# Kernel optimization log

Measured on AMD Instinct MI355X. Metric: run time of the kernel, lower is better.

The kernel has to match this reference:

```python
import jax, jax.numpy as jnp
import numpy as np
from jax import lax

K = 17  # depthwise conv kernel size (MossFormer ConvModule)
DIM = 512
HID = 2048      # dim * expansion_factor(4)
DQK = 128
GRP = 256       # group_size


def layernorm(x, g, b, eps=1e-5):
    mu = x.mean(-1, keepdims=True)
    var = ((x - mu) ** 2).mean(-1, keepdims=True)
    return (x - mu) * lax.rsqrt(var + eps) * g + b


def dwconv_res(h, dw):
    # h: [b, n, c]; dw: [K, c] depthwise kernel; residual connection, SAME padding
    c = h.shape[-1]
    conv = lax.conv_general_dilated(h, dw[:, None, :], (1,), 'SAME',
                                    dimension_numbers=('NWC', 'WIO', 'NWC'),
                                    feature_group_count=c)
    return h + conv


def ffconvm(x, ln_g, ln_b, W, b, dw):
    h = jax.nn.silu(layernorm(x, ln_g, ln_b) @ W + b)
    return dwconv_res(h, dw)


def setup_inputs() -> dict:
    key = jax.random.key(0)
    ks = jax.random.split(key, 16)
    r = lambda k, shape, s=0.02: (jax.random.normal(k, shape, dtype=jnp.float32) * s)
    inp = {
        'x': jax.random.normal(ks[0], (8, 2048, DIM), dtype=jnp.float32),
        # to_hidden FFConvM: LN(dim) -> Linear(dim, HID) -> SiLU -> depthwise conv residual
        'ln_h_g': jnp.ones((DIM,), jnp.float32), 'ln_h_b': jnp.zeros((DIM,), jnp.float32),
        'W_h': r(ks[1], (DIM, HID)), 'b_h': jnp.zeros((HID,), jnp.float32),
        'dw_h': r(ks[2], (K, HID)),
        # to_qk FFConvM: LN(dim) -> Linear(dim, DQK) -> SiLU -> conv residual
        'ln_qk_g': jnp.ones((DIM,), jnp.float32), 'ln_qk_b': jnp.zeros((DIM,), jnp.float32),
        'W_qk': r(ks[3], (DIM, DQK)), 'b_qk': jnp.zeros((DQK,), jnp.float32),
        'dw_qk': r(ks[4], (K, DQK)),
        # OffsetScale: gamma ~ N(0, 0.02) offset... torch init: gamma = 1 + small noise? source: ones then normal_(std=0.02) overwrites -> N(0,0.02); beta zeros
        'gamma': r(ks[5], (4, DQK)),
        'beta': jnp.zeros((4, DQK), jnp.float32),
        # to_out FFConvM: LN(2*dim) -> Linear(2*dim, dim) -> SiLU -> conv residual
        'ln_o_g': jnp.ones((2 * DIM,), jnp.float32), 'ln_o_b': jnp.zeros((2 * DIM,), jnp.float32),
        'W_o': r(ks[6], (2 * DIM, DIM)), 'b_o': jnp.zeros((DIM,), jnp.float32),
        'dw_o': r(ks[7], (K, DIM)),
    }
    return inp


def reference(x, ln_h_g, ln_h_b, W_h, b_h, dw_h,
              ln_qk_g, ln_qk_b, W_qk, b_qk, dw_qk,
              gamma, beta,
              ln_o_g, ln_o_b, W_o, b_o, dw_o):
    b, n, d = x.shape
    g = GRP
    # shift tokens: shift first half of channels forward by one step
    x1, x2 = jnp.split(x, 2, axis=-1)
    x1 = jnp.pad(x1, ((0, 0), (1, 0), (0, 0)))[:, :n]
    nx = jnp.concatenate([x1, x2], axis=-1)

    hid = ffconvm(nx, ln_h_g, ln_h_b, W_h, b_h, dw_h)       # [b,n,HID]
    v, u = jnp.split(hid, 2, axis=-1)                        # each [b,n,HID/2]
    qk = ffconvm(nx, ln_qk_g, ln_qk_b, W_qk, b_qk, dw_qk)    # [b,n,DQK]

    qk4 = qk[..., None, :] * gamma + beta                    # [b,n,4,DQK]
    quad_q, lin_q, quad_k, lin_k = (qk4[..., i, :] for i in range(4))

    G = n // g  # n chosen divisible by group_size (no padding path)
    grp = lambda t: t.reshape(b, G, g, t.shape[-1])
    quad_q, quad_k, lin_q, lin_k, vg, ug = map(grp, (quad_q, quad_k, lin_q, lin_k, v, u))

    # grouped quadratic attention: relu^2, causal within group
    sim = jnp.einsum('bgid,bgjd->bgij', quad_q, quad_k) / g
    attn = jnp.square(jax.nn.relu(sim))
    causal_mask = jnp.triu(jnp.ones((g, g), dtype=bool), 1)
    attn = jnp.where(causal_mask, 0.0, attn)
    quad_v = jnp.einsum('bgij,bgje->bgie', attn, vg)
    quad_u = jnp.einsum('bgij,bgje->bgie', attn, ug)

    # linear attention across groups with causal cumsum over the group dim
    lin_kv = jnp.einsum('bgnd,bgne->bgde', lin_k, vg) / g
    lin_kv = jnp.pad(jnp.cumsum(lin_kv, axis=1), ((0, 0), (1, 0), (0, 0), (0, 0)))[:, :G]
    lin_v = jnp.einsum('bgde,bgnd->bgne', lin_kv, lin_q)
    lin_ku = jnp.einsum('bgnd,bgne->bgde', lin_k, ug) / g
    lin_ku = jnp.pad(jnp.cumsum(lin_ku, axis=1), ((0, 0), (1, 0), (0, 0), (0, 0)))[:, :G]
    lin_u = jnp.einsum('bgde,bgnd->bgne', lin_ku, lin_q)

    att_v = (quad_v + lin_v).reshape(b, n, -1)
    att_u = (quad_u + lin_u).reshape(b, n, -1)

    out = att_u * v * jax.nn.sigmoid(att_v * u)              # [b,n,2*dim]
    return x + ffconvm(out, ln_o_g, ln_o_b, W_o, b_o, dw_o)
```

## Files before the change

### kernel.cpp

```cpp
#include <hip/hip_runtime.h>
#include <hip/hip_bf16.h>

typedef __hip_bfloat16 bf16;
typedef __attribute__((ext_vector_type(8))) short short8;
typedef __attribute__((ext_vector_type(4))) short short4v;
typedef __attribute__((ext_vector_type(2))) short short2v;
typedef __attribute__((ext_vector_type(4))) float float4v;
typedef __attribute__((ext_vector_type(2))) float float2v;
__device__ __forceinline__ float b2f(bf16 v){ return __bfloat162float(v); }
__device__ __forceinline__ bf16 f2b(float v){ return __float2bfloat16(v); }
__device__ __forceinline__ void stv(float* p, long i, float v){ p[i] = v; }
__device__ __forceinline__ void stv(bf16*  p, long i, float v){ p[i] = f2b(v); }

#define MFMA __builtin_amdgcn_mfma_f32_16x16x32_bf16
#define AS1(p) ((const __attribute__((address_space(1))) void*)(p))
#define AS3(p) ((__attribute__((address_space(3))) void*)(p))

#define BB   8
#define NN   2048
#define DIM  512
#define HID  2048
#define DQK  128
#define GRP  256
#define NG   8
#define KW   17
#define BK   32
#define NHQ  2176

template<int D, int SHIFT_HALF>
__global__ __launch_bounds__(256) void ln_kernel_f(const float* __restrict__ in,
                                                   bf16* __restrict__ out)
{
    int row = blockIdx.x;
    int t = row % NN;
    int tid = threadIdx.x;
    int c0 = tid * 2;
    float2v v2 = {0.f, 0.f};
    if (SHIFT_HALF && c0 < D / 2) {
        if (t > 0) v2 = *(const float2v*)(in + ((long)row - 1) * D + c0);
    } else {
        v2 = *(const float2v*)(in + (long)row * D + c0);
    }
    float s = v2[0] + v2[1];
    float ss = v2[0] * v2[0] + v2[1] * v2[1];
    for (int o = 32; o > 0; o >>= 1) { s += __shfl_down(s, o); ss += __shfl_down(ss, o); }
    __shared__ float sm[4], sm2[4];
    int wid = tid >> 6, lane = tid & 63;
    if (lane == 0) { sm[wid] = s; sm2[wid] = ss; }
    __syncthreads();
    if (tid == 0) {
        float a = 0.f, q = 0.f;
        for (int w = 0; w < 4; w++) { a += sm[w]; q += sm2[w]; }
        sm[0] = a; sm2[0] = q;
    }
    __syncthreads();
    float mean = sm[0] / D;
    float var  = fmaxf(sm2[0] / D - mean * mean, 0.f);
    float rs = rsqrtf(var + 1e-5f);
    union { short2v v; bf16 h[2]; } o2;
    o2.h[0] = f2b((v2[0] - mean) * rs);
    o2.h[1] = f2b((v2[1] - mean) * rs);
    *(short2v*)(out + (long)row * D + c0) = o2.v;
}

template<int D>
__global__ __launch_bounds__(256) void ln_kernel_bf(const bf16* __restrict__ in,
                                                    bf16* __restrict__ out)
{
    int row = blockIdx.x;
    int tid = threadIdx.x;
    int c0 = tid * 4;
    union { short4v v; bf16 h[4]; } u;
    u.v = *(const short4v*)(in + (long)row * D + c0);
    float vals[4];
    float s = 0.f, ss = 0.f;
    #pragma unroll
    for (int i = 0; i < 4; i++) {
        float v = b2f(u.h[i]);
        vals[i] = v; s += v; ss += v * v;
    }
    for (int o = 32; o > 0; o >>= 1) { s += __shfl_down(s, o); ss += __shfl_down(ss, o); }
    __shared__ float sm[4], sm2[4];
    int wid = tid >> 6, lane = tid & 63;
    if (lane == 0) { sm[wid] = s; sm2[wid] = ss; }
    __syncthreads();
    if (tid == 0) {
        float a = 0.f, q = 0.f;
        for (int w = 0; w < 4; w++) { a += sm[w]; q += sm2[w]; }
        sm[0] = a; sm2[0] = q;
    }
    __syncthreads();
    float mean = sm[0] / D;
    float var  = fmaxf(sm2[0] / D - mean * mean, 0.f);
    float rs = rsqrtf(var + 1e-5f);
    union { short4v v; bf16 h[4]; } o4;
    #pragma unroll
    for (int i = 0; i < 4; i++) o4.h[i] = f2b((vals[i] - mean) * rs);
    *(short4v*)(out + (long)row * D + c0) = o4.v;
}

__global__ __launch_bounds__(256) void prep_all(
    const float* __restrict__ W_h,  const float* __restrict__ g_h,  bf16* __restrict__ WT_h,
    const float* __restrict__ W_qk, const float* __restrict__ g_qk, bf16* __restrict__ WT_qk,
    const float* __restrict__ W_o,  const float* __restrict__ g_o,  bf16* __restrict__ WT_o)
{
    int i = blockIdx.x;
    const float *W, *g; bf16* WT; int K, N, k0, n0;
    if (i < 1024) {
        W = W_h; g = g_h; WT = WT_h; K = DIM; N = HID;
        k0 = (i & 15) * 32; n0 = (i >> 4) * 32;
    } else if (i < 1088) {
        int j = i - 1024;
        W = W_qk; g = g_qk; WT = WT_qk; K = DIM; N = DQK;
        k0 = (j & 15) * 32; n0 = (j >> 4) * 32;
    } else {
        int j = i - 1088;
        W = W_o; g = g_o; WT = WT_o; K = 1024; N = DIM;
        k0 = (j & 31) * 32; n0 = (j >> 5) * 32;
    }
    __shared__ float Ws[32][33];
    int tid = threadIdx.x;
    for (int l = 0; l < 4; l++) {
        int e = tid + 256 * l;
        int kk = e >> 5, nn = e & 31;
        Ws[kk][nn] = g[k0 + kk] * W[(size_t)(k0 + kk) * N + n0 + nn];
    }
    __syncthreads();
    for (int l = 0; l < 4; l++) {
        int e = tid + 256 * l;
        int nn = e >> 5, kk = e & 31;
        WT[(size_t)(n0 + nn) * K + k0 + kk] = f2b(Ws[kk][nn]);
    }
}

__global__ __launch_bounds__(256) void bias_init3(
    const float* __restrict__ b_h, const float* __restrict__ b_qk,
    const float* __restrict__ b_o, float* __restrict__ out)
{
    int n = blockIdx.x * 256 + threadIdx.x;
    if (n < HID)            out[n] = b_h[n];
    else if (n < NHQ)       out[n] = b_qk[n - HID];
    else if (n < NHQ + DIM) out[n] = b_o[n - NHQ];
}

#define BKC 64
__global__ __launch_bounds__(256) void bias_reduce3(
    const float* __restrict__ W_h,  const float* __restrict__ lnb_h,
    const float* __restrict__ W_qk, const float* __restrict__ lnb_qk,
    const float* __restrict__ W_o,  const float* __restrict__ lnb_o,
    float* __restrict__ bias_hq, float* __restrict__ bias_o)
{
    int i = blockIdx.x;
    const float *W, *lnb; float* out; int N, n, k0;
    if (i < 64) {
        W = W_h; lnb = lnb_h; out = bias_hq; N = HID;
        n = (i & 7) * 256 + threadIdx.x; k0 = (i >> 3) * BKC;
    } else if (i < 72) {
        int j = i - 64;
        W = W_qk; lnb = lnb_qk; out = bias_hq + HID; N = DQK;
        n = threadIdx.x; k0 = j * BKC;
    } else {
        int j = i - 72;
        W = W_o; lnb = lnb_o; out = bias_o; N = DIM;
        n = (j & 1) * 256 + threadIdx.x; k0 = (j >> 1) * BKC;
    }
    if (n >= N) return;
    float s = 0.f;
    #pragma unroll 8
    for (int k = k0; k < k0 + BKC; k++) s += lnb[k] * W[(size_t)k * N + n];
    atomicAdd(&out[n], s);
}

__device__ __forceinline__ void stage_tile(const bf16* base, size_t ld, bf16* dst,
                                           int wave, int lane)
{
    int lrow = lane >> 2, lcol = lane & 3;
    for (int cc = 0; cc < 2; cc++) {
        int c = wave * 2 + cc;
        int row = c * 16 + lrow;
        const bf16* g = base + (size_t)row * ld + lcol * 8;
        __builtin_amdgcn_global_load_lds(AS1(g), AS3(dst + c * 512), 16, 0, 0);
    }
}

#define PIPE_SLOT 8192

__device__ __forceinline__ void pipe_core(
    const bf16* __restrict__ Abase, size_t ldA,
    const bf16* __restrict__ Bbase, size_t ldB,
    int nit, bf16* lds, int wave, int lane, float4v acc[4][4])
{
    auto stage = [&](int it, int slot) {
        bf16* As = lds + slot * PIPE_SLOT;
        stage_tile(Abase + (size_t)it * 32, ldA, As, wave, lane);
        stage_tile(Bbase + (size_t)it * 32, ldB, As + 4096, wave, lane);
    };
    stage(0, 0);
    stage(1, 1);
    asm volatile("s_waitcnt vmcnt(4)" ::: "memory");
    __builtin_amdgcn_s_barrier();
    __builtin_amdgcn_sched_barrier(0);

    int wm = wave & 1, wn = wave >> 1;
    int col = lane & 15, quad = lane >> 4;
    int slot = 0;
    for (int it = 0; it < nit; it++) {
        const bf16* As = lds + slot * PIPE_SLOT;
        const bf16* Bs = As + 4096;
        short8 a[4], b[4];
        #pragma unroll
        for (int t = 0; t < 4; t++) {
            a[t] = *(const short8*)(As + (wm * 64 + t * 16 + col) * 32 + quad * 8);
            b[t] = *(const short8*)(Bs + (wn * 64 + t * 16 + col) * 32 + quad * 8);
        }
        int nslot = slot + 1; if (nslot == 3) nslot = 0;
        int pslot = nslot + 1; if (pslot == 3) pslot = 0;
        if (it + 2 < nit) stage(it + 2, pslot);
        asm volatile("s_waitcnt lgkmcnt(0)" ::: "memory");
        __builtin_amdgcn_sched_barrier(0);
        __builtin_amdgcn_s_setprio(1);
        #pragma unroll
        for (int i = 0; i < 4; i++)
            #pragma unroll
            for (int j = 0; j < 4; j++)
                acc[i][j] = MFMA(a[i], b[j], acc[i][j], 0, 0, 0);
        __builtin_amdgcn_s_setprio(0);
        __builtin_amdgcn_sched_barrier(0);
        if (it + 2 < nit) { asm volatile("s_waitcnt vmcnt(4)" ::: "memory"); }
        else              { asm volatile("s_waitcnt vmcnt(0)" ::: "memory"); }
        __builtin_amdgcn_s_barrier();
        __builtin_amdgcn_sched_barrier(0);
        slot = nslot;
    }
}

__global__ __launch_bounds__(256) void gemm_pipe(
    const bf16* __restrict__ A, const bf16* __restrict__ BT,
    const float* __restrict__ bias, bf16* __restrict__ C,
    int M, int N, int K, int ldC)
{
    __shared__ __align__(16) bf16 lds[3 * PIPE_SLOT];
    int nb = N >> 7;
    int i = blockIdx.x;
    int xcd = i & 7, r = i >> 3;
    int m0 = (xcd + 8 * (r / nb)) << 7;
    int n0 = (r % nb) << 7;
    int tid = threadIdx.x, wave = tid >> 6, lane = tid & 63;
    float4v acc[4][4] = {};
    pipe_core(A + (size_t)m0 * K, K, BT + (size_t)n0 * K, K, K / 32,
              lds, wave, lane, acc);
    int wm = wave & 1, wn = wave >> 1;
    int col = lane & 15, quad = lane >> 4;
    for (int i2 = 0; i2 < 4; i2++) {
        for (int j = 0; j < 4; j++) {
            int n = n0 + wn * 64 + j * 16 + col;
            float bs = bias[n];
            for (int r2 = 0; r2 < 4; r2++) {
                int m = m0 + wm * 64 + i2 * 16 + quad * 4 + r2;
                float v = acc[i2][j][r2] + bs;
                v = v / (1.f + __expf(-v));
                C[(size_t)m * ldC + n] = f2b(v);
            }
        }
    }
}

__device__ __forceinline__ void stage_half256(const bf16* __restrict__ g0, int ld,
                                              bf16* dst, int tid)
{
    int wb = tid & ~63;
    #pragma unroll
    for (int l = 0; l < 2; l++) {
        int idx = l * 512 + tid;
        int row = idx >> 3;
        int c8  = (idx & 7) ^ (row & 7);
        const bf16* g = g0 + (size_t)row * ld + c8 * 8;
        __builtin_amdgcn_global_load_lds(AS1(g), AS3(dst + (size_t)(l * 512 + wb) * 8), 16, 0, 0);
    }
}

__device__ __forceinline__ short8 ldsfrag(const bf16* h, int row, int g)
{
    return *(const short8*)(h + row * 64 + ((g ^ (row & 7)) << 3));
}

__global__ __launch_bounds__(512, 2) void gemm256(
    const bf16* __restrict__ A, const bf16* __restrict__ BT,
    const float* __restrict__ bias, bf16* __restrict__ C,
    int N, int K, int ldC)
{
    __shared__ __align__(16) bf16 As[2][2][128][64];
    __shared__ __align__(16) bf16 Bs[2][2][128][64];
    int nbx = N >> 8;
    int nwg = gridDim.x;
    int cpx = nwg >> 3;
    int bid = blockIdx.x;
    int swz = (bid & 7) * cpx + (bid >> 3);
    int bx = swz % nbx, by = swz / nbx;
    int m0 = by << 8, n0 = bx << 8;
    int tid = threadIdx.x, wave = tid >> 6, lane = tid & 63;
    int wm = wave >> 2, wn = wave & 3;
    int col = lane & 15, quad = lane >> 4;
    int nkt = K >> 6;
    float4v acc[8][4] = {};

    const bf16* Ag = A  + (size_t)m0 * K;
    const bf16* Bg = BT + (size_t)n0 * K;

    #pragma unroll
    for (int h = 0; h < 2; h++) {
        stage_half256(Ag + (size_t)h * 128 * K, K, &As[0][h][0][0], tid);
        stage_half256(Bg + (size_t)h * 128 * K, K, &Bs[0][h][0][0], tid);
    }
    asm volatile("s_waitcnt vmcnt(0)" ::: "memory");
    __builtin_amdgcn_s_barrier();

    for (int kt = 0; kt < nkt; kt++) {
        int buf = kt & 1;
        const bf16* Ah = &As[buf][wm][0][0];
        const bf16* Bh = &Bs[buf][wn >> 1][0][0];
        int brb = (wn & 1) * 64;
        short8 ar[2][4], br[2][2], br2[2][2];
        bool pf = (kt + 1 < nkt);

        #pragma unroll
        for (int i = 0; i < 4; i++)
            #pragma unroll
            for (int ks = 0; ks < 2; ks++)
                ar[ks][i] = ldsfrag(Ah, i * 16 + col, ks * 4 + quad);
        #pragma unroll
        for (int j = 0; j < 2; j++)
            #pragma unroll
            for (int ks = 0; ks < 2; ks++)
                br[ks][j] = ldsfrag(Bh, brb + j * 16 + col, ks * 4 + quad);
        if (pf) {
            #pragma unroll
            for (int h = 0; h < 2; h++) {
                stage_half256(Ag + (size_t)h * 128 * K + (kt + 1) * 64, K,
                              &As[buf ^ 1][h][0][0], tid);
                stage_half256(Bg + (size_t)h * 128 * K + (kt + 1) * 64, K,
                              &Bs[buf ^ 1][h][0][0], tid);
            }
        }
        __builtin_amdgcn_s_barrier();
        __builtin_amdgcn_s_setprio(1);
        #pragma unroll
        for (int i = 0; i < 4; i++)
            #pragma unroll
            for (int j = 0; j < 2; j++) {
                acc[i][j] = MFMA(ar[0][i], br[0][j], acc[i][j], 0, 0, 0);
                acc[i][j] = MFMA(ar[1][i], br[1][j], acc[i][j], 0, 0, 0);
            }
        __builtin_amdgcn_s_setprio(0);
        __builtin_amdgcn_s_barrier();

        #pragma unroll
        for (int j = 0; j < 2; j++)
            #pragma unroll
            for (int ks = 0; ks < 2; ks++)
                br2[ks][j] = ldsfrag(Bh, brb + (j + 2) * 16 + col, ks * 4 + quad);
        __builtin_amdgcn_s_barrier();
        __builtin_amdgcn_s_setprio(1);
        #pragma unroll
        for (int i = 0; i < 4; i++)
            #pragma unroll
            for (int j = 0; j < 2; j++) {
                acc[i][j + 2] = MFMA(ar[0][i], br2[0][j], acc[i][j + 2], 0, 0, 0);
                acc[i][j + 2] = MFMA(ar[1][i], br2[1][j], acc[i][j + 2], 0, 0, 0);
            }
        __builtin_amdgcn_s_setprio(0);
        __builtin_amdgcn_s_barrier();

        #pragma unroll
        for (int i = 0; i < 4; i++)
            #pragma unroll
            for (int ks = 0; ks < 2; ks++)
                ar[ks][i] = ldsfrag(Ah, (i + 4) * 16 + col, ks * 4 + quad);
        __builtin_amdgcn_s_barrier();
        __builtin_amdgcn_s_setprio(1);
        #pragma unroll
        for (int i = 0; i < 4; i++)
            #pragma unroll
            for (int j = 0; j < 2; j++) {
                acc[i + 4][j + 2] = MFMA(ar[0][i], br2[0][j], acc[i + 4][j + 2], 0, 0, 0);
                acc[i + 4][j + 2] = MFMA(ar[1][i], br2[1][j], acc[i + 4][j + 2], 0, 0, 0);
            }
        __builtin_amdgcn_s_setprio(0);
        __builtin_amdgcn_s_barrier();

        #pragma unroll
        for (int j = 0; j < 2; j++)
            #pragma unroll
            for (int ks = 0; ks < 2; ks++)
                br[ks][j] = ldsfrag(Bh, brb + j * 16 + col, ks * 4 + quad);
        __builtin_amdgcn_s_barrier();
        __builtin_amdgcn_s_setprio(1);
        #pragma unroll
        for (int i = 0; i < 4; i++)
            #pragma unroll
            for (int j = 0; j < 2; j++) {
                acc[i + 4][j] = MFMA(ar[0][i], br[0][j], acc[i + 4][j], 0, 0, 0);
                acc[i + 4][j] = MFMA(ar[1][i], br[1][j], acc[i + 4][j], 0, 0, 0);
            }
        __builtin_amdgcn_s_setprio(0);
        __builtin_amdgcn_sched_barrier(0);
        asm volatile("s_waitcnt vmcnt(0)" ::: "memory");
        __builtin_amdgcn_s_barrier();
    }

    #pragma unroll
    for (int i = 0; i < 8; i++) {
        #pragma unroll
        for (int j = 0; j < 4; j++) {
            int n = n0 + wn * 64 + j * 16 + col;
            float bs = bias[n];
            #pragma unroll
            for (int r = 0; r < 4; r++) {
                int m = m0 + wm * 128 + i * 16 + quad * 4 + r;
                float v = acc[i][j][r] + bs;
                v = v / (1.f + __expf(-v));
                C[(size_t)m * ldC + n] = f2b(v);
            }
        }
    }
}

__global__ __launch_bounds__(256) void score_linkv(
    const bf16* __restrict__ quadq, const bf16* __restrict__ quadk,
    bf16* __restrict__ P,
    const bf16* __restrict__ hidT, const bf16* __restrict__ linkT,
    float* __restrict__ linkvT, int rowsC, int nScore)
{
    __shared__ __align__(16) bf16 lds[3 * PIPE_SLOT];
    int tid = threadIdx.x, wave = tid >> 6, lane = tid & 63;
    if ((int)blockIdx.x < nScore) {
        int i = blockIdx.x;
        int xcd = i & 7, r = i >> 3;
        int g = xcd + 8 * (r >> 2);
        int t = r & 3, bi = t >> 1, bj = t & 1;
        bf16* Pg = P + (size_t)g * GRP * GRP;
        if (bj > bi) {
            short8 z = {};
            int rr = tid >> 1, half = tid & 1;
            short* dst = (short*)Pg + (size_t)(bi * 128 + rr) * GRP + bj * 128 + half * 64;
            for (int q = 0; q < 8; q++) ((short8*)dst)[q] = z;
            return;
        }
        float4v acc[4][4] = {};
        const bf16* Ab = quadq + (size_t)(g * GRP + bi * 128) * DQK;
        const bf16* Bb = quadk + (size_t)(g * GRP + bj * 128) * DQK;
        pipe_core(Ab, DQK, Bb, DQK, DQK / 32, lds, wave, lane, acc);
        int wm = wave & 1, wn = wave >> 1;
        int col = lane & 15, quad = lane >> 4;
        for (int i2 = 0; i2 < 4; i2++) {
            for (int j = 0; j < 4; j++) {
                int jj = bj * 128 + wn * 64 + j * 16 + col;
                for (int r2 = 0; r2 < 4; r2++) {
                    int ii = bi * 128 + wm * 64 + i2 * 16 + quad * 4 + r2;
                    float s = acc[i2][j][r2] * (1.f / GRP);
                    s = fmaxf(s, 0.f); s = s * s;
                    if (jj > ii) s = 0.f;
                    Pg[(size_t)ii * GRP + jj] = f2b(s);
                }
            }
        }
    } else {
        int i = blockIdx.x - nScore;
        int xcd = i & 7, r = i >> 3;
        int g = xcd + 8 * (r >> 4);
        int eb = r & 15;
        int e0 = eb * 128;
        float4v acc[4][4] = {};
        pipe_core(hidT + (size_t)e0 * rowsC + g * GRP, rowsC,
                  linkT + g * GRP, rowsC, GRP / 32, lds, wave, lane, acc);
        float* out = linkvT + (size_t)g * (HID * DQK);
        int wm = wave & 1, wn = wave >> 1;
        int col = lane & 15, quad = lane >> 4;
        for (int i2 = 0; i2 < 4; i2++) {
            for (int j = 0; j < 4; j++) {
                int d = wn * 64 + j * 16 + col;
                for (int r2 = 0; r2 < 4; r2++) {
                    int e = e0 + wm * 64 + i2 * 16 + quad * 4 + r2;
                    out[(size_t)e * DQK + d] = acc[i2][j][r2] * (1.f / GRP);
                }
            }
        }
    }
}

__global__ void cumsum_bf(const float* __restrict__ in, bf16* __restrict__ out)
{
    long idx4 = (long)blockIdx.x * blockDim.x + threadIdx.x;
    int b = (int)(idx4 / (DQK * HID / 4));
    long off = (idx4 % (DQK * HID / 4)) * 4;
    const float* pi = in + (long)b * NG * DQK * HID + off;
    bf16* po = out + (long)b * NG * DQK * HID + off;
    float4v run = {0.f, 0.f, 0.f, 0.f};
    for (int gi = 0; gi < NG; gi++) {
        short4v o4;
        union { short s; bf16 h; } cv;
        #pragma unroll
        for (int k = 0; k < 4; k++) { cv.h = f2b(run[k]); o4[k] = cv.s; }
        *(short4v*)(po + (long)gi * DQK * HID) = o4;
        run += *(const float4v*)(pi + (long)gi * DQK * HID);
    }
}

#define AP_SLOT (256 * BK + 128 * BK)

__global__ __launch_bounds__(256) void attn_apply_mfma(
    const bf16* __restrict__ P, const bf16* __restrict__ hidT,
    const bf16* __restrict__ linq, const bf16* __restrict__ linkvb,
    const bf16* __restrict__ hid, bf16* __restrict__ outg, int rowsC)
{
    int ib = blockIdx.x;
    int xcd = ib & 7, rb = ib >> 3;
    int g = xcd + 8 * (rb >> 4);
    int e0 = (rb & 15) * 64;
    __shared__ __align__(16) bf16 lds[3 * AP_SLOT];
    int tid = threadIdx.x, wave = tid >> 6, lane = tid & 63;
    int lrow = lane >> 2, lcol = lane & 3;
    const bf16* Pg = P + (size_t)g * GRP * GRP;
    const bf16* Lg = linkvb + (size_t)g * (HID * DQK);

    auto stage = [&](int it, int slot) {
        bf16* As = lds + slot * AP_SLOT;
        bf16* Bs = As + 256 * BK;
        if (it < 8) {
            int j0 = it * 32;
            for (int cc = 0; cc < 4; cc++) {
                int c = wave * 4 + cc;
                int row = c * 16 + lrow;
                const bf16* ga = Pg + (size_t)row * GRP + j0 + lcol * 8;
                __builtin_amdgcn_global_load_lds(AS1(ga), AS3(As + c * 512), 16, 0, 0);
            }
            for (int cc = 0; cc < 2; cc++) {
                int c = wave * 2 + cc;
                int row = c * 16 + lrow;
                int er = (row < 64) ? (e0 + row) : (1024 + e0 + (row - 64));
                const bf16* gb = hidT + (size_t)er * rowsC + g * GRP + j0 + lcol * 8;
                __builtin_amdgcn_global_load_lds(AS1(gb), AS3(Bs + c * 512), 16, 0, 0);
            }
        } else {
            int d0 = (it - 8) * 32;
            for (int cc = 0; cc < 4; cc++) {
                int c = wave * 4 + cc;
                int row = c * 16 + lrow;
                const bf16* ga = linq + (size_t)(g * GRP + row) * DQK + d0 + lcol * 8;
                __builtin_amdgcn_global_load_lds(AS1(ga), AS3(As + c * 512), 16, 0, 0);
            }
            for (int cc = 0; cc < 2; cc++) {
                int c = wave * 2 + cc;
                int row = c * 16 + lrow;
                int er = (row < 64) ? (e0 + row) : (1024 + e0 + (row - 64));
                const bf16* gb = Lg + (size_t)er * DQK + d0 + lcol * 8;
                __builtin_amdgcn_global_load_lds(AS1(gb), AS3(Bs + c * 512), 16, 0, 0);
            }
        }
    };

    stage(0, 0);
    stage(1, 1);
    asm volatile("s_waitcnt vmcnt(6)" ::: "memory");
    __builtin_amdgcn_s_barrier();
    __builtin_amdgcn_sched_barrier(0);

    float4v acc[4][8] = {};
    int col = lane & 15, quad = lane >> 4;
    int slot = 0;
    for (int it = 0; it < 12; it++) {
        const bf16* As = lds + slot * AP_SLOT;
        const bf16* Bs = As + 256 * BK;
        short8 a[4], b[8];
        #pragma unroll
        for (int t = 0; t < 4; t++)
            a[t] = *(const short8*)(As + (wave * 64 + t * 16 + col) * BK + quad * 8);
        #pragma unroll
        for (int t = 0; t < 8; t++)
            b[t] = *(const short8*)(Bs + (t * 16 + col) * BK + quad * 8);
        int nslot = slot + 1; if (nslot == 3) nslot = 0;
        int pslot = nslot + 1; if (pslot == 3) pslot = 0;
        if (it + 2 < 12) stage(it + 2, pslot);
        asm volatile("s_waitcnt lgkmcnt(0)" ::: "memory");
        __builtin_amdgcn_sched_barrier(0);
        __builtin_amdgcn_s_setprio(1);
        #pragma unroll
        for (int i = 0; i < 4; i++)
            #pragma unroll
            for (int j = 0; j < 8; j++)
                acc[i][j] = MFMA(a[i], b[j], acc[i][j], 0, 0, 0);
        __builtin_amdgcn_s_setprio(0);
        __builtin_amdgcn_sched_barrier(0);
        if (it + 2 < 12) { asm volatile("s_waitcnt vmcnt(6)" ::: "memory"); }
        else             { asm volatile("s_waitcnt vmcnt(0)" ::: "memory"); }
        __builtin_amdgcn_s_barrier();
        __builtin_amdgcn_sched_barrier(0);
        slot = nslot;
    }

    for (int mt = 0; mt < 4; mt++) {
        for (int nt = 0; nt < 4; nt++) {
            for (int r = 0; r < 4; r++) {
                int tokg = g * GRP + wave * 64 + mt * 16 + quad * 4 + r;
                int e = e0 + nt * 16 + col;
                float av = acc[mt][nt][r];
                float au = acc[mt][nt + 4][r];
                float v = b2f(hid[(size_t)tokg * HID + e]);
                float u = b2f(hid[(size_t)tokg * HID + 1024 + e]);
                float gate = 1.f / (1.f + __expf(-av * u));
                outg[(size_t)tokg * 1024 + e] = f2b(au * v * gate);
            }
        }
    }
}

__global__ __launch_bounds__(256) void dwconv_both(
    const bf16* __restrict__ hq, const float* __restrict__ dw_h,
    bf16* __restrict__ hid, bf16* __restrict__ hidT,
    const float* __restrict__ dw_qk,
    const float* __restrict__ gamma, const float* __restrict__ beta,
    bf16* __restrict__ quadq, bf16* __restrict__ quadk,
    bf16* __restrict__ linq, bf16* __restrict__ linkT,
    int rowsC, int nDual)
{
    __shared__ float s[80][64];
    __shared__ bf16 o[64][72];
    int tid = threadIdx.x;
    if ((int)blockIdx.x < nDual) {
        int i = blockIdx.x;
        int c0 = (i & 31) * 64;
        int t0 = ((i >> 5) & 31) * 64;
        int b  = i >> 10;
        const bf16* base = hq + (size_t)b * NN * NHQ + c0;
        {
            int ch8 = (tid & 7) * 8, rw = tid >> 3;
            #pragma unroll
            for (int ps = 0; ps < 3; ps++) {
                int tt = rw + ps * 32;
                if (tt < 80) {
                    int t = t0 + tt - 8;
                    union { short8 v; bf16 h[8]; } u; u.v = short8{};
                    if (t >= 0 && t < NN)
                        u.v = *(const short8*)(base + (size_t)t * NHQ + ch8);
                    float* sp = &s[tt][ch8];
                    #pragma unroll
                    for (int k = 0; k < 8; k++) sp[k] = b2f(u.h[k]);
                }
            }
        }
        __syncthreads();
        int c = tid & 63, rp = tid >> 6;
        float w[KW];
        for (int k = 0; k < KW; k++) w[k] = dw_h[k * HID + c0 + c];
        for (int l = 0; l < 16; l++) {
            int r = rp + l * 4;
            float acc = s[r + 8][c];
            for (int k = 0; k < KW; k++) acc += s[r + k][c] * w[k];
            o[c][r] = f2b(acc);
        }
        __syncthreads();
        {
            int ch8 = (tid & 7) * 8, rw = tid >> 3;
            #pragma unroll
            for (int ps = 0; ps < 2; ps++) {
                int r = rw + ps * 32;
                union { short8 v; bf16 h[8]; } u;
                #pragma unroll
                for (int k = 0; k < 8; k++) u.h[k] = o[ch8 + k][r];
                *(short8*)(hid + ((size_t)b * NN + t0 + r) * HID + c0 + ch8) = u.v;
            }
        }
        {
            int t8 = (tid & 7) * 8, ch = tid >> 3;
            #pragma unroll
            for (int ps = 0; ps < 2; ps++) {
                int cc = ch + ps * 32;
                short8 v = *(const short8*)(&o[cc][t8]);
                *(short8*)(hidT + (size_t)(c0 + cc) * rowsC + b * NN + t0 + t8) = v;
            }
        }
    } else {
        int i = blockIdx.x - nDual;
        int c0 = (i & 1) * 64;
        int t0 = ((i >> 1) & 31) * 64;
        int b  = i >> 6;
        const bf16* base = hq + HID + (size_t)b * NN * NHQ + c0;
        {
            int ch8 = (tid & 7) * 8, rw = tid >> 3;
            #pragma unroll
            for (int ps = 0; ps < 3; ps++) {
                int tt = rw + ps * 32;
                if (tt < 80) {
                    int t = t0 + tt - 8;
                    union { short8 v; bf16 h[8]; } u; u.v = short8{};
                    if (t >= 0 && t < NN)
                        u.v = *(const short8*)(base + (size_t)t * NHQ + ch8);
                    float* sp = &s[tt][ch8];
                    #pragma unroll
                    for (int k = 0; k < 8; k++) sp[k] = b2f(u.h[k]);
                }
            }
        }
        __syncthreads();
        int c = tid & 63, rp = tid >> 6;
        float w[KW];
        for (int k = 0; k < KW; k++) w[k] = dw_qk[k * DQK + c0 + c];
        float ga0 = gamma[0 * DQK + c0 + c], be0 = beta[0 * DQK + c0 + c];
        float ga1 = gamma[1 * DQK + c0 + c], be1 = beta[1 * DQK + c0 + c];
        float ga2 = gamma[2 * DQK + c0 + c], be2 = beta[2 * DQK + c0 + c];
        float ga3 = gamma[3 * DQK + c0 + c], be3 = beta[3 * DQK + c0 + c];
        for (int l = 0; l < 16; l++) {
            int r = rp + l * 4;
            float acc = s[r + 8][c];
            for (int k = 0; k < KW; k++) acc += s[r + k][c] * w[k];
            size_t tok = (size_t)b * NN + t0 + r;
            quadq[tok * DQK + c0 + c] = f2b(acc * ga0 + be0);
            linq [tok * DQK + c0 + c] = f2b(acc * ga1 + be1);
            quadk[tok * DQK + c0 + c] = f2b(acc * ga2 + be2);
            o[c][r] = f2b(acc * ga3 + be3);
        }
        __syncthreads();
        int t8 = (tid & 7) * 8, ch = tid >> 3;
        #pragma unroll
        for (int ps = 0; ps < 2; ps++) {
            int cc = ch + ps * 32;
            short8 v = *(const short8*)(&o[cc][t8]);
            *(short8*)(linkT + (size_t)(c0 + cc) * rowsC + b * NN + t0 + t8) = v;
        }
    }
}

template<typename TO>
__global__ __launch_bounds__(256) void dwconv_res(
    const bf16* __restrict__ src, const float* __restrict__ dw,
    const float* __restrict__ xres, TO* __restrict__ dst, int C, int ldS)
{
    int c0 = blockIdx.x * 64;
    int t0 = blockIdx.y * 64;
    int b  = blockIdx.z;
    __shared__ float s[80][64];
    int tid = threadIdx.x;
    int c = tid & 63;
    int rp = tid >> 6;
    const bf16* base = src + (size_t)b * NN * ldS + c0;
    {
        int ch8 = (tid & 7) * 8, rw = tid >> 3;
        #pragma unroll
        for (int ps = 0; ps < 3; ps++) {
            int tt = rw + ps * 32;
            if (tt < 80) {
                int t = t0 + tt - 8;
                union { short8 v; bf16 h[8]; } u; u.v = short8{};
                if (t >= 0 && t < NN)
                    u.v = *(const short8*)(base + (size_t)t * ldS + ch8);
                float* sp = &s[tt][ch8];
                #pragma unroll
                for (int k = 0; k < 8; k++) sp[k] = b2f(u.h[k]);
            }
        }
    }
    __syncthreads();
    float w[KW];
    for (int k = 0; k < KW; k++) w[k] = dw[k * C + c0 + c];
    for (int l = 0; l < 16; l++) {
        int r = rp + l * 4;
        float acc = s[r + 8][c];
        for (int k = 0; k < KW; k++) acc += s[r + k][c] * w[k];
        long gidx = ((long)b * NN + t0 + r) * C + c0 + c;
        if (xres) acc += xres[gidx];
        stv(dst, gidx, acc);
    }
}

extern "C" void kernel_launch(void* const* d_in, const int* in_sizes, int n_in,
                              void* d_out, int out_size, void* d_ws, size_t ws_size,
                              hipStream_t stream)
{
    const float* x      = (const float*)d_in[0];
    const float* ln_h_g = (const float*)d_in[1];
    const float* ln_h_b = (const float*)d_in[2];
    const float* W_h    = (const float*)d_in[3];
    const float* b_h    = (const float*)d_in[4];
    const float* dw_h   = (const float*)d_in[5];
    const float* ln_qk_g= (const float*)d_in[6];
    const float* ln_qk_b= (const float*)d_in[7];
    const float* W_qk   = (const float*)d_in[8];
    const float* b_qk   = (const float*)d_in[9];
    const float* dw_qk  = (const float*)d_in[10];
    const float* gamma  = (const float*)d_in[11];
    const float* beta   = (const float*)d_in[12];
    const float* ln_o_g = (const float*)d_in[13];
    const float* ln_o_b = (const float*)d_in[14];
    const float* W_o    = (const float*)d_in[15];
    const float* b_o    = (const float*)d_in[16];
    const float* dw_o   = (const float*)d_in[17];
    float* outp = (float*)d_out;

    char* p = (char*)d_ws;
    bf16* WT_hq = (bf16*)p;  p += (size_t)NHQ * DIM * 2;
    bf16* WT_o  = (bf16*)p;  p += (size_t)DIM * 1024 * 2;
    float* bias_hq = (float*)p; p += NHQ * 4;
    float* bias_o  = (float*)p; p += DIM * 4;
    p = (char*)(((uintptr_t)p + 255) & ~(uintptr_t)255);
    size_t fixed = (size_t)(p - (char*)d_ws);
    bf16* WT_h  = WT_hq;
    bf16* WT_qk = WT_hq + (size_t)HID * DIM;
    float* bias_h  = bias_hq;

    auto bytes_for = [fixed](int cb) -> size_t {
        size_t rows = (size_t)cb * NN;
        return fixed
             + rows * NHQ * 2
             + rows * HID * 2
             + rows * HID * 2
             + rows * 1024 * 2
             + rows * DIM * 2
             + 5 * rows * DQK * 2
             + rows * 1024 * 2
             + 4096;
    };
    int CB = 1;
    if (bytes_for(4) <= ws_size) CB = 4;
    else if (bytes_for(2) <= ws_size) CB = 2;
    const int rowsC = CB * NN;
    const size_t rows = (size_t)rowsC;

    char* s1 = p;               p += rows * NHQ * 2;
    char* s2 = p;               p += rows * HID * 2;
    char* s3 = p;               p += rows * HID * 2;
    char* s4 = p;               p += rows * 1024 * 2;
    char* s5 = p;               p += rows * DIM * 2;
    char* s6 = p;               p += rows * DQK * 2;
    char* s7 = p;               p += rows * DQK * 2;
    char* s8 = p;               p += rows * DQK * 2;
    char* s9 = p;               p += rows * DQK * 2;
    char* s10 = p;              p += rows * DQK * 2;
    char* s11 = p;              p += rows * 1024 * 2;

    bf16*  hq      = (bf16*)s1;
    float* linkvT  = (float*)s1;
    bf16*  fin_pre = (bf16*)s1;
    bf16*  hid     = (bf16*)s2;
    bf16*  hat2    = (bf16*)s2;
    bf16*  hidT    = (bf16*)s3;
    bf16*  outg    = (bf16*)s4;
    bf16*  hat1    = (bf16*)s5;
    bf16*  P       = (bf16*)s5;
    bf16*  linkT   = (bf16*)s6;
    (void)s7;
    bf16*  quadq   = (bf16*)s8;
    bf16*  quadk   = (bf16*)s9;
    bf16*  linq    = (bf16*)s10;
    bf16*  linkvb  = (bf16*)s11;

    prep_all<<<1600, 256, 0, stream>>>(W_h, ln_h_g, WT_h,
                                       W_qk, ln_qk_g, WT_qk,
                                       W_o, ln_o_g, WT_o);
    bias_init3<<<(NHQ + DIM + 255) / 256, 256, 0, stream>>>(b_h, b_qk, b_o, bias_hq);
    bias_reduce3<<<104, 256, 0, stream>>>(W_h, ln_h_b, W_qk, ln_qk_b, W_o, ln_o_b,
                                          bias_hq, bias_o);

    const int G = CB * NG;
    for (int b0 = 0; b0 < BB; b0 += CB) {
        const float* xc = x    + (size_t)b0 * NN * DIM;
        float* outc     = outp + (size_t)b0 * NN * DIM;
        int R = rowsC;

        ln_kernel_f<DIM, 1><<<R, 256, 0, stream>>>(xc, hat1);
        gemm256<<<dim3((R / 256) * (HID / 256)), 512, 0, stream>>>(
            hat1, WT_h, bias_h, hq, HID, DIM, NHQ);
        gemm_pipe<<<dim3((R / 128) * 1), 256, 0, stream>>>(
            hat1, WT_qk, bias_hq + HID, hq + HID, R, 128, DIM, NHQ);
        {
            int nDual = (HID / 64) * (NN / 64) * CB;
            int nQk   = (DQK / 64) * (NN / 64) * CB;
            dwconv_both<<<nDual + nQk, 256, 0, stream>>>(
                hq, dw_h, hid, hidT, dw_qk, gamma, beta,
                quadq, quadk, linq, linkT, rowsC, nDual);
        }
        score_linkv<<<4 * G + 16 * G, 256, 0, stream>>>(
            quadq, quadk, P, hidT, linkT, linkvT, rowsC, 4 * G);
        cumsum_bf<<<(CB * DQK * HID) / (256 * 4), 256, 0, stream>>>(linkvT, linkvb);
        attn_apply_mfma<<<dim3(16 * G), 256, 0, stream>>>(P, hidT, linq, linkvb, hid, outg, rowsC);
        ln_kernel_bf<1024><<<R, 256, 0, stream>>>(outg, hat2);
        gemm_pipe<<<dim3((DIM / 128) * (R / 128)), 256, 0, stream>>>(
            hat2, WT_o, bias_o, fin_pre, R, DIM, 1024, DIM);
        dwconv_res<float><<<dim3(DIM / 64, NN / 64, CB), 256, 0, stream>>>(
            fin_pre, dw_o, xc, outc, DIM, DIM);
    }
}
```

Baseline: 452.8 us.

## Merge hidden and qk projections into one padded GEMM and drop row-major hid copy

Pads the fused hidden+qk weight matrix to 2304 columns (zero-filled bias) so a single gemm256 launch computes both projections, replacing the separate gemm_pipe launch for qk. The depthwise conv kernel no longer writes the row-major hid buffer; attn_apply reads v/u from the transposed hidT instead, with token-strided access. The input layernorm is hoisted out of the batch-chunk loop into one launch over all rows, and workspace buffers are resized accordingly. The padded columns add wasted GEMM work, and the transposed gather in the epilogue may be less coalesced.

```diff
diff --git a/kernel.cpp b/kernel.cpp
--- a/kernel.cpp
+++ b/kernel.cpp
@@ -26,6 +26,7 @@
 #define KW   17
 #define BK   32
 #define NHQ  2176
+#define NHQ2 2304
 
 template<int D, int SHIFT_HALF>
 __global__ __launch_bounds__(256) void ln_kernel_f(const float* __restrict__ in,
@@ -135,12 +136,14 @@
 
 __global__ __launch_bounds__(256) void bias_init3(
     const float* __restrict__ b_h, const float* __restrict__ b_qk,
-    const float* __restrict__ b_o, float* __restrict__ out)
+    const float* __restrict__ b_o, float* __restrict__ bias_hq,
+    float* __restrict__ bias_o)
 {
     int n = blockIdx.x * 256 + threadIdx.x;
-    if (n < HID)            out[n] = b_h[n];
-    else if (n < NHQ)       out[n] = b_qk[n - HID];
-    else if (n < NHQ + DIM) out[n] = b_o[n - NHQ];
+    if (n < HID)                 bias_hq[n] = b_h[n];
+    else if (n < NHQ)            bias_hq[n] = b_qk[n - HID];
+    else if (n < NHQ2)           bias_hq[n] = 0.f;
+    else if (n < NHQ2 + DIM)     bias_o[n - NHQ2] = b_o[n - NHQ2];
 }
 
 #define BKC 64
@@ -511,7 +514,7 @@
 __global__ __launch_bounds__(256) void attn_apply_mfma(
     const bf16* __restrict__ P, const bf16* __restrict__ hidT,
     const bf16* __restrict__ linq, const bf16* __restrict__ linkvb,
-    const bf16* __restrict__ hid, bf16* __restrict__ outg, int rowsC)
+    bf16* __restrict__ outg, int rowsC)
 {
     int ib = blockIdx.x;
     int xcd = ib & 7, rb = ib >> 3;
@@ -605,8 +608,8 @@
                 int e = e0 + nt * 16 + col;
                 float av = acc[mt][nt][r];
                 float au = acc[mt][nt + 4][r];
-                float v = b2f(hid[(size_t)tokg * HID + e]);
-                float u = b2f(hid[(size_t)tokg * HID + 1024 + e]);
+                float v = b2f(hidT[(size_t)e * rowsC + tokg]);
+                float u = b2f(hidT[(size_t)(1024 + e) * rowsC + tokg]);
                 float gate = 1.f / (1.f + __expf(-av * u));
                 outg[(size_t)tokg * 1024 + e] = f2b(au * v * gate);
             }
@@ -616,7 +619,7 @@
 
 __global__ __launch_bounds__(256) void dwconv_both(
     const bf16* __restrict__ hq, const float* __restrict__ dw_h,
-    bf16* __restrict__ hid, bf16* __restrict__ hidT,
+    bf16* __restrict__ hidT,
     const float* __restrict__ dw_qk,
     const float* __restrict__ gamma, const float* __restrict__ beta,
     bf16* __restrict__ quadq, bf16* __restrict__ quadk,
@@ -631,7 +634,7 @@
         int c0 = (i & 31) * 64;
         int t0 = ((i >> 5) & 31) * 64;
         int b  = i >> 10;
-        const bf16* base = hq + (size_t)b * NN * NHQ + c0;
+        const bf16* base = hq + (size_t)b * NN * NHQ2 + c0;
         {
             int ch8 = (tid & 7) * 8, rw = tid >> 3;
             #pragma unroll
@@ -641,7 +644,7 @@
                     int t = t0 + tt - 8;
                     union { short8 v; bf16 h[8]; } u; u.v = short8{};
                     if (t >= 0 && t < NN)
-                        u.v = *(const short8*)(base + (size_t)t * NHQ + ch8);
+                        u.v = *(const short8*)(base + (size_t)t * NHQ2 + ch8);
                     float* sp = &s[tt][ch8];
                     #pragma unroll
                     for (int k = 0; k < 8; k++) sp[k] = b2f(u.h[k]);
@@ -660,17 +663,6 @@
         }
         __syncthreads();
         {
-            int ch8 = (tid & 7) * 8, rw = tid >> 3;
-            #pragma unroll
-            for (int ps = 0; ps < 2; ps++) {
-                int r = rw + ps * 32;
-                union { short8 v; bf16 h[8]; } u;
-                #pragma unroll
-                for (int k = 0; k < 8; k++) u.h[k] = o[ch8 + k][r];
-                *(short8*)(hid + ((size_t)b * NN + t0 + r) * HID + c0 + ch8) = u.v;
-            }
-        }
-        {
             int t8 = (tid & 7) * 8, ch = tid >> 3;
             #pragma unroll
             for (int ps = 0; ps < 2; ps++) {
@@ -684,7 +676,7 @@
         int c0 = (i & 1) * 64;
         int t0 = ((i >> 1) & 31) * 64;
         int b  = i >> 6;
-        const bf16* base = hq + HID + (size_t)b * NN * NHQ + c0;
+        const bf16* base = hq + HID + (size_t)b * NN * NHQ2 + c0;
         {
             int ch8 = (tid & 7) * 8, rw = tid >> 3;
             #pragma unroll
@@ -694,7 +686,7 @@
                     int t = t0 + tt - 8;
                     union { short8 v; bf16 h[8]; } u; u.v = short8{};
                     if (t >= 0 && t < NN)
-                        u.v = *(const short8*)(base + (size_t)t * NHQ + ch8);
+                        u.v = *(const short8*)(base + (size_t)t * NHQ2 + ch8);
                     float* sp = &s[tt][ch8];
                     #pragma unroll
                     for (int k = 0; k < 8; k++) sp[k] = b2f(u.h[k]);
@@ -797,10 +789,11 @@
     float* outp = (float*)d_out;
 
     char* p = (char*)d_ws;
-    bf16* WT_hq = (bf16*)p;  p += (size_t)NHQ * DIM * 2;
+    bf16* WT_hq = (bf16*)p;  p += (size_t)NHQ2 * DIM * 2;
     bf16* WT_o  = (bf16*)p;  p += (size_t)DIM * 1024 * 2;
-    float* bias_hq = (float*)p; p += NHQ * 4;
+    float* bias_hq = (float*)p; p += NHQ2 * 4;
     float* bias_o  = (float*)p; p += DIM * 4;
+    bf16* hat1_all = (bf16*)p;  p += (size_t)BB * NN * DIM * 2;
     p = (char*)(((uintptr_t)p + 255) & ~(uintptr_t)255);
     size_t fixed = (size_t)(p - (char*)d_ws);
     bf16* WT_h  = WT_hq;
@@ -810,12 +803,12 @@
     auto bytes_for = [fixed](int cb) -> size_t {
         size_t rows = (size_t)cb * NN;
         return fixed
-             + rows * NHQ * 2
-             + rows * HID * 2
+             + rows * NHQ2 * 2
+             + rows * 1024 * 2
              + rows * HID * 2
              + rows * 1024 * 2
-             + rows * DIM * 2
-             + 5 * rows * DQK * 2
+             + (size_t)cb * NG * GRP * GRP * 2
+             + 4 * rows * DQK * 2
              + rows * 1024 * 2
              + 4096;
     };
@@ -825,13 +818,12 @@
     const int rowsC = CB * NN;
     const size_t rows = (size_t)rowsC;
 
-    char* s1 = p;               p += rows * NHQ * 2;
-    char* s2 = p;               p += rows * HID * 2;
+    char* s1 = p;               p += rows * NHQ2 * 2;
+    char* s2 = p;               p += rows * 1024 * 2;
     char* s3 = p;               p += rows * HID * 2;
     char* s4 = p;               p += rows * 1024 * 2;
-    char* s5 = p;               p += rows * DIM * 2;
+    char* s5 = p;               p += (size_t)CB * NG * GRP * GRP * 2;
     char* s6 = p;               p += rows * DQK * 2;
-    char* s7 = p;               p += rows * DQK * 2;
     char* s8 = p;               p += rows * DQK * 2;
     char* s9 = p;               p += rows * DQK * 2;
     char* s10 = p;              p += rows * DQK * 2;
@@ -840,14 +832,11 @@
     bf16*  hq      = (bf16*)s1;
     float* linkvT  = (float*)s1;
     bf16*  fin_pre = (bf16*)s1;
-    bf16*  hid     = (bf16*)s2;
     bf16*  hat2    = (bf16*)s2;
     bf16*  hidT    = (bf16*)s3;
     bf16*  outg    = (bf16*)s4;
-    bf16*  hat1    = (bf16*)s5;
     bf16*  P       = (bf16*)s5;
     bf16*  linkT   = (bf16*)s6;
-    (void)s7;
     bf16*  quadq   = (bf16*)s8;
     bf16*  quadk   = (bf16*)s9;
     bf16*  linq    = (bf16*)s10;
@@ -856,32 +845,31 @@
     prep_all<<<1600, 256, 0, stream>>>(W_h, ln_h_g, WT_h,
                                        W_qk, ln_qk_g, WT_qk,
                                        W_o, ln_o_g, WT_o);
-    bias_init3<<<(NHQ + DIM + 255) / 256, 256, 0, stream>>>(b_h, b_qk, b_o, bias_hq);
+    bias_init3<<<(NHQ2 + DIM + 255) / 256, 256, 0, stream>>>(b_h, b_qk, b_o, bias_hq, bias_o);
     bias_reduce3<<<104, 256, 0, stream>>>(W_h, ln_h_b, W_qk, ln_qk_b, W_o, ln_o_b,
                                           bias_hq, bias_o);
+    ln_kernel_f<DIM, 1><<<BB * NN, 256, 0, stream>>>(x, hat1_all);
 
     const int G = CB * NG;
     for (int b0 = 0; b0 < BB; b0 += CB) {
         const float* xc = x    + (size_t)b0 * NN * DIM;
         float* outc     = outp + (size_t)b0 * NN * DIM;
+        const bf16* hat1 = hat1_all + (size_t)b0 * NN * DIM;
         int R = rowsC;
 
-        ln_kernel_f<DIM, 1><<<R, 256, 0, stream>>>(xc, hat1);
-        gemm256<<<dim3((R / 256) * (HID / 256)), 512, 0, stream>>>(
-            hat1, WT_h, bias_h, hq, HID, DIM, NHQ);
-        gemm_pipe<<<dim3((R / 128) * 1), 256, 0, stream>>>(
-            hat1, WT_qk, bias_hq + HID, hq + HID, R, 128, DIM, NHQ);
+        gemm256<<<dim3((R / 256) * (NHQ2 / 256)), 512, 0, stream>>>(
+            hat1, WT_hq, bias_hq, hq, NHQ2, DIM, NHQ2);
         {
             int nDual = (HID / 64) * (NN / 64) * CB;
             int nQk   = (DQK / 64) * (NN / 64) * CB;
             dwconv_both<<<nDual + nQk, 256, 0, stream>>>(
-                hq, dw_h, hid, hidT, dw_qk, gamma, beta,
+                hq, dw_h, hidT, dw_qk, gamma, beta,
                 quadq, quadk, linq, linkT, rowsC, nDual);
         }
         score_linkv<<<4 * G + 16 * G, 256, 0, stream>>>(
             quadq, quadk, P, hidT, linkT, linkvT, rowsC, 4 * G);
         cumsum_bf<<<(CB * DQK * HID) / (256 * 4), 256, 0, stream>>>(linkvT, linkvb);
-        attn_apply_mfma<<<dim3(16 * G), 256, 0, stream>>>(P, hidT, linq, linkvb, hid, outg, rowsC);
+        attn_apply_mfma<<<dim3(16 * G), 256, 0, stream>>>(P, hidT, linq, linkvb, outg, rowsC);
         ln_kernel_bf<1024><<<R, 256, 0, stream>>>(outg, hat2);
         gemm_pipe<<<dim3((DIM / 128) * (R / 128)), 256, 0, stream>>>(
             hat2, WT_o, bias_o, fin_pre, R, DIM, 1024, DIM);
```

Measured after the change: 460.6 us. Within noise of the previous version (+1.7%).
